# Kernel tuning notes

Hardware: AMD Instinct MI355X
Metric: run time of the kernel (lower is better)

## Reference

```python
import jax, jax.numpy as jnp
import numpy as np

MARGIN = 0.3
EPS = 1e-12


def setup_inputs() -> dict:
    key = jax.random.key(0)
    k1, k2 = jax.random.split(key)
    inputs = jax.random.normal(k1, (128, 131072), dtype=jnp.float32)
    targets = jax.random.randint(k2, (128,), 0, 8).astype(jnp.int64)
    return {"inputs": inputs, "targets": targets}


def reference(inputs, targets):
    n = inputs.shape[0]  # 128, hardcoded layout: two modality halves of 64
    # Pairwise Euclidean distance matrix (n, n)
    sq = jnp.sum(inputs * inputs, axis=1, keepdims=True)  # (n, 1)
    dist = sq + sq.T - 2.0 * (inputs @ inputs.T)
    dist = jnp.sqrt(jnp.clip(dist, EPS, None))

    same_label = targets[:, None] == targets[None, :]  # (n, n)
    # modality indicator: first half = modality 0, second half = modality 1
    half = jnp.arange(n) >= (n // 2)
    cross_modality = half[:, None] != half[None, :]  # (n, n)

    # hard positive: same label, opposite modality (mask * mask_modality_final)
    pos_mask = same_label & cross_modality
    # hard negative: where (mask + mask_modality_final_neg) == 0
    # i.e. different label AND opposite modality
    neg_mask = (~same_label) & cross_modality

    neg_inf = jnp.float32(-jnp.inf)
    pos_inf = jnp.float32(jnp.inf)
    dist_ap = jnp.max(jnp.where(pos_mask, dist, neg_inf), axis=1)  # (n,)
    dist_an = jnp.min(jnp.where(neg_mask, dist, pos_inf), axis=1)  # (n,)

    # MarginRankingLoss with y=1: mean(relu(-(dist_an - dist_ap) + margin))
    loss = jnp.mean(jax.nn.relu(dist_ap - dist_an + MARGIN))
    return loss
```

## Files before the change

kernel.cpp:

```cpp
#include <hip/hip_runtime.h>
#include <hip/hip_bf16.h>

typedef __attribute__((ext_vector_type(8))) short  bf16x8;
typedef __attribute__((ext_vector_type(8))) ushort ushortx8;
typedef __attribute__((ext_vector_type(4))) float  f32x4;

#define N     128
#define KTOT  131072
#define NB    256
#define KC    (KTOT / NB)
#define BK    64
#define NST   (KC / BK)
#define LDT   72

__device__ __forceinline__ ushort f2bf(float f) {
    union { float f; unsigned u; } v; v.f = f;
    const unsigned u = v.u;
    return (ushort)((u + 0x7fffu + ((u >> 16) & 1u)) >> 16);
}

template <bool ATOMIC>
__global__ __launch_bounds__(512) void gram_kernel(const float* __restrict__ X,
                                                   float* __restrict__ out) {
    __shared__ ushort tile[N][LDT];

    const int t    = threadIdx.x;
    const int lane = t & 63;
    const int wv   = t >> 6;
    const int fr   = lane & 15;
    const int fh   = lane >> 4;
    const int r0   = t >> 4;
    const int c4   = t & 15;

    const long kbase = (long)blockIdx.x * KC;
    const float* xp = X + kbase + (long)r0 * KTOT + c4 * 4;

    f32x4 acc[8];
#pragma unroll
    for (int j = 0; j < 8; ++j) acc[j] = (f32x4){0.f, 0.f, 0.f, 0.f};

    float4 rg[4], ng[4];
#pragma unroll
    for (int p = 0; p < 4; ++p)
        rg[p] = *(const float4*)(xp + (long)(32 * p) * KTOT);

    auto store_stage = [&]() {
#pragma unroll
        for (int p = 0; p < 4; ++p) {
            ushort4 h;
            h.x = f2bf(rg[p].x); h.y = f2bf(rg[p].y);
            h.z = f2bf(rg[p].z); h.w = f2bf(rg[p].w);
            *(ushort4*)&tile[r0 + 32 * p][c4 * 4] = h;
        }
    };
    auto mfma_stage = [&]() {
#pragma unroll
        for (int kh = 0; kh < 2; ++kh) {
            const bf16x8 af = *(const bf16x8*)&tile[wv * 16 + fr][kh * 32 + fh * 8];
#pragma unroll
            for (int j = 0; j < 8; ++j) {
                const bf16x8 bf = *(const bf16x8*)&tile[j * 16 + fr][kh * 32 + fh * 8];
                acc[j] = __builtin_amdgcn_mfma_f32_16x16x32_bf16(af, bf, acc[j], 0, 0, 0);
            }
        }
    };

    for (int s = 0; s < NST - 1; ++s) {
        __syncthreads();
        store_stage();
#pragma unroll
        for (int p = 0; p < 4; ++p)
            ng[p] = *(const float4*)(xp + (long)(s + 1) * BK + (long)(32 * p) * KTOT);
        __syncthreads();
        mfma_stage();
#pragma unroll
        for (int p = 0; p < 4; ++p) rg[p] = ng[p];
    }
    __syncthreads();
    store_stage();
    __syncthreads();
    mfma_stage();

    if (ATOMIC) {
#pragma unroll
        for (int j = 0; j < 8; ++j)
#pragma unroll
            for (int r = 0; r < 4; ++r)
                atomicAdd(&out[(wv * 16 + fh * 4 + r) * N + j * 16 + fr], acc[j][r]);
    } else {
        float* dst = out + (size_t)blockIdx.x * (size_t)(N * N);
#pragma unroll
        for (int j = 0; j < 8; ++j)
#pragma unroll
            for (int r = 0; r < 4; ++r)
                dst[(wv * 16 + fh * 4 + r) * N + j * 16 + fr] = acc[j][r];
    }
}

__global__ __launch_bounds__(256) void reduce_kernel(const float* __restrict__ part,
                                                     float* __restrict__ C) {
    __shared__ float2 red[256];
    const int t  = threadIdx.x;
    const int g  = t >> 5;
    const int jo = t & 31;
    const size_t jb = (size_t)blockIdx.x * 64;

    float2 s = {0.f, 0.f};
#pragma unroll 8
    for (int b = 0; b < 32; ++b) {
        const float2 v = ((const float2*)(part + (size_t)(g * 32 + b) * (N * N) + jb))[jo];
        s.x += v.x; s.y += v.y;
    }
    red[t] = s;
    __syncthreads();
    if (t < 32) {
        float2 a = red[t];
#pragma unroll
        for (int g2 = 1; g2 < 8; ++g2) {
            const float2 v = red[g2 * 32 + t];
            a.x += v.x; a.y += v.y;
        }
        ((float2*)(C + jb))[t] = a;
    }
}

__global__ __launch_bounds__(128) void loss_kernel(const float* __restrict__ C,
                                                   const int* __restrict__ tg,
                                                   float* __restrict__ out) {
    __shared__ float Cs[N][N + 4];
    __shared__ float sqs[N];
    __shared__ int   ts[N];
    __shared__ float red[2];

    const int t = threadIdx.x;
#pragma unroll
    for (int it = 0; it < 32; ++it) {
        const int idx = it * 512 + t * 4;
        const float4 v = *(const float4*)(C + idx);
        const int r = idx >> 7;
        const int c = idx & 127;
        Cs[r][c] = v.x; Cs[r][c + 1] = v.y; Cs[r][c + 2] = v.z; Cs[r][c + 3] = v.w;
    }
    ts[t] = tg[t];
    __syncthreads();
    sqs[t] = Cs[t][t];
    __syncthreads();

    const int   ti  = ts[t];
    const int   hi  = t >> 6;
    const float sqi = sqs[t];
    float ap = -INFINITY, an = INFINITY;
#pragma unroll 4
    for (int jj = 0; jj < N; ++jj) {
        const int j = (jj + t) & (N - 1);
        const float d2 = sqi + sqs[j] - 2.0f * Cs[t][j];
        const float d  = sqrtf(fmaxf(d2, 1e-12f));
        const bool cross = ((j >> 6) != hi);
        const bool same  = (ts[j] == ti);
        if (cross && same)  ap = fmaxf(ap, d);
        if (cross && !same) an = fminf(an, d);
    }
    float li = fmaxf(ap - an + 0.3f, 0.0f);

#pragma unroll
    for (int off = 32; off > 0; off >>= 1)
        li += __shfl_down(li, off, 64);
    if ((t & 63) == 0) red[t >> 6] = li;
    __syncthreads();
    if (t == 0) out[0] = (red[0] + red[1]) * (1.0f / (float)N);
}

extern "C" void kernel_launch(void* const* d_in, const int* in_sizes, int n_in,
                              void* d_out, int out_size, void* d_ws, size_t ws_size,
                              hipStream_t stream) {
    const float* X   = (const float*)d_in[0];
    const int*   tg  = (const int*)d_in[1];
    float*       out = (float*)d_out;

    const size_t part_elems = (size_t)NB * (size_t)(N * N);
    const size_t need       = (part_elems + (size_t)(N * N)) * sizeof(float);

    if (ws_size >= need) {
        float* part = (float*)d_ws;
        float* C    = part + part_elems;
        gram_kernel<false><<<NB, 512, 0, stream>>>(X, part);
        reduce_kernel<<<(N * N) / 64, 256, 0, stream>>>(part, C);
        loss_kernel<<<1, 128, 0, stream>>>(C, tg, out);
    } else {
        float* C = (float*)d_ws;
        hipMemsetAsync(C, 0, (size_t)(N * N) * sizeof(float), stream);
        gram_kernel<true><<<NB, 512, 0, stream>>>(X, C);
        loss_kernel<<<1, 128, 0, stream>>>(C, tg, out);
    }
}
```

Before: 111.1 us.

## Double-buffer LDS tiles with two-deep prefetch and split loss rows across threads

The gram kernel now keeps two LDS tile buffers and prefetches global data two stages ahead, which removes one barrier per K-stage and gives loads more time to arrive before use. The loop is fully unrolled. The loss kernel doubles its thread count so each row's 128 column scan is split in half, and the two partial max/min results are merged through shared memory. In exchange the kernel holds more registers for prefetch, doubles LDS use, and unrolling all 8 stages grows the code.

```diff
diff --git a/kernel.cpp b/kernel.cpp
--- a/kernel.cpp
+++ b/kernel.cpp
@@ -2,7 +2,6 @@
 #include <hip/hip_bf16.h>
 
 typedef __attribute__((ext_vector_type(8))) short  bf16x8;
-typedef __attribute__((ext_vector_type(8))) ushort ushortx8;
 typedef __attribute__((ext_vector_type(4))) float  f32x4;
 
 #define N     128
@@ -22,7 +21,7 @@
 template <bool ATOMIC>
 __global__ __launch_bounds__(512) void gram_kernel(const float* __restrict__ X,
                                                    float* __restrict__ out) {
-    __shared__ ushort tile[N][LDT];
+    __shared__ ushort tile[2][N][LDT];
 
     const int t    = threadIdx.x;
     const int lane = t & 63;
@@ -39,47 +38,38 @@
 #pragma unroll
     for (int j = 0; j < 8; ++j) acc[j] = (f32x4){0.f, 0.f, 0.f, 0.f};
 
-    float4 rg[4], ng[4];
+    float4 pf[2][4];
 #pragma unroll
-    for (int p = 0; p < 4; ++p)
-        rg[p] = *(const float4*)(xp + (long)(32 * p) * KTOT);
+    for (int p = 0; p < 4; ++p) pf[0][p] = *(const float4*)(xp + (long)(32 * p) * KTOT);
+#pragma unroll
+    for (int p = 0; p < 4; ++p) pf[1][p] = *(const float4*)(xp + BK + (long)(32 * p) * KTOT);
 
-    auto store_stage = [&]() {
+#pragma unroll
+    for (int s = 0; s < NST; ++s) {
+        const int cur = s & 1;
 #pragma unroll
         for (int p = 0; p < 4; ++p) {
             ushort4 h;
-            h.x = f2bf(rg[p].x); h.y = f2bf(rg[p].y);
-            h.z = f2bf(rg[p].z); h.w = f2bf(rg[p].w);
-            *(ushort4*)&tile[r0 + 32 * p][c4 * 4] = h;
+            h.x = f2bf(pf[cur][p].x); h.y = f2bf(pf[cur][p].y);
+            h.z = f2bf(pf[cur][p].z); h.w = f2bf(pf[cur][p].w);
+            *(ushort4*)&tile[cur][r0 + 32 * p][c4 * 4] = h;
         }
-    };
-    auto mfma_stage = [&]() {
+        if (s + 2 < NST) {
+#pragma unroll
+            for (int p = 0; p < 4; ++p)
+                pf[cur][p] = *(const float4*)(xp + (long)(s + 2) * BK + (long)(32 * p) * KTOT);
+        }
+        __syncthreads();
 #pragma unroll
         for (int kh = 0; kh < 2; ++kh) {
-            const bf16x8 af = *(const bf16x8*)&tile[wv * 16 + fr][kh * 32 + fh * 8];
+            const bf16x8 af = *(const bf16x8*)&tile[cur][wv * 16 + fr][kh * 32 + fh * 8];
 #pragma unroll
             for (int j = 0; j < 8; ++j) {
-                const bf16x8 bf = *(const bf16x8*)&tile[j * 16 + fr][kh * 32 + fh * 8];
+                const bf16x8 bf = *(const bf16x8*)&tile[cur][j * 16 + fr][kh * 32 + fh * 8];
                 acc[j] = __builtin_amdgcn_mfma_f32_16x16x32_bf16(af, bf, acc[j], 0, 0, 0);
             }
         }
-    };
-
-    for (int s = 0; s < NST - 1; ++s) {
-        __syncthreads();
-        store_stage();
-#pragma unroll
-        for (int p = 0; p < 4; ++p)
-            ng[p] = *(const float4*)(xp + (long)(s + 1) * BK + (long)(32 * p) * KTOT);
-        __syncthreads();
-        mfma_stage();
-#pragma unroll
-        for (int p = 0; p < 4; ++p) rg[p] = ng[p];
     }
-    __syncthreads();
-    store_stage();
-    __syncthreads();
-    mfma_stage();
 
     if (ATOMIC) {
 #pragma unroll
@@ -124,48 +114,56 @@
     }
 }
 
-__global__ __launch_bounds__(128) void loss_kernel(const float* __restrict__ C,
+__global__ __launch_bounds__(256) void loss_kernel(const float* __restrict__ C,
                                                    const int* __restrict__ tg,
                                                    float* __restrict__ out) {
     __shared__ float Cs[N][N + 4];
     __shared__ float sqs[N];
     __shared__ int   ts[N];
+    __shared__ float aph[N], anh[N];
     __shared__ float red[2];
 
     const int t = threadIdx.x;
 #pragma unroll
-    for (int it = 0; it < 32; ++it) {
-        const int idx = it * 512 + t * 4;
+    for (int it = 0; it < 16; ++it) {
+        const int idx = it * 1024 + t * 4;
         const float4 v = *(const float4*)(C + idx);
         const int r = idx >> 7;
         const int c = idx & 127;
         Cs[r][c] = v.x; Cs[r][c + 1] = v.y; Cs[r][c + 2] = v.z; Cs[r][c + 3] = v.w;
     }
-    ts[t] = tg[t];
+    if (t < N) ts[t] = tg[t];
     __syncthreads();
-    sqs[t] = Cs[t][t];
+    if (t < N) sqs[t] = Cs[t][t];
     __syncthreads();
 
-    const int   ti  = ts[t];
-    const int   hi  = t >> 6;
-    const float sqi = sqs[t];
+    const int   r   = t & 127;
+    const int   h2  = t >> 7;
+    const int   ti  = ts[r];
+    const int   hi  = r >> 6;
+    const float sqi = sqs[r];
     float ap = -INFINITY, an = INFINITY;
 #pragma unroll 4
-    for (int jj = 0; jj < N; ++jj) {
-        const int j = (jj + t) & (N - 1);
-        const float d2 = sqi + sqs[j] - 2.0f * Cs[t][j];
+    for (int jj = 0; jj < 64; ++jj) {
+        const int j = h2 * 64 + ((jj + r) & 63);
+        const float d2 = sqi + sqs[j] - 2.0f * Cs[r][j];
         const float d  = sqrtf(fmaxf(d2, 1e-12f));
         const bool cross = ((j >> 6) != hi);
         const bool same  = (ts[j] == ti);
         if (cross && same)  ap = fmaxf(ap, d);
         if (cross && !same) an = fminf(an, d);
     }
-    float li = fmaxf(ap - an + 0.3f, 0.0f);
-
+    if (h2) { aph[r] = ap; anh[r] = an; }
+    __syncthreads();
+    if (!h2) {
+        ap = fmaxf(ap, aph[r]);
+        an = fminf(an, anh[r]);
+        float li = fmaxf(ap - an + 0.3f, 0.0f);
 #pragma unroll
-    for (int off = 32; off > 0; off >>= 1)
-        li += __shfl_down(li, off, 64);
-    if ((t & 63) == 0) red[t >> 6] = li;
+        for (int off = 32; off > 0; off >>= 1)
+            li += __shfl_down(li, off, 64);
+        if ((r & 63) == 0) red[r >> 6] = li;
+    }
     __syncthreads();
     if (t == 0) out[0] = (red[0] + red[1]) * (1.0f / (float)N);
 }
@@ -185,11 +183,11 @@
         float* C    = part + part_elems;
         gram_kernel<false><<<NB, 512, 0, stream>>>(X, part);
         reduce_kernel<<<(N * N) / 64, 256, 0, stream>>>(part, C);
-        loss_kernel<<<1, 128, 0, stream>>>(C, tg, out);
+        loss_kernel<<<1, 256, 0, stream>>>(C, tg, out);
     } else {
         float* C = (float*)d_ws;
         hipMemsetAsync(C, 0, (size_t)(N * N) * sizeof(float), stream);
         gram_kernel<true><<<NB, 512, 0, stream>>>(X, C);
-        loss_kernel<<<1, 128, 0, stream>>>(C, tg, out);
+        loss_kernel<<<1, 256, 0, stream>>>(C, tg, out);
     }
 }
```

New measurement: 103.2 us. -7.2%, faster.
